# Kernel tuning notes

Hardware: AMD Instinct MI355X
Metric: run time of the kernel (lower is better)

## Reference

```python
import jax, jax.numpy as jnp
import numpy as np


def setup_inputs() -> dict:
    key = jax.random.key(0)
    k1, k2, k3, k4 = jax.random.split(key, 4)
    b, c, h, w = 16, 1024, 32, 32
    dim = h * w  # 1024
    x = jax.random.normal(k1, (b, c, h, w), dtype=jnp.float32)
    cond_img = jax.random.normal(k2, (b, c, h, w), dtype=jnp.float32)
    # torch nn.Linear weights: (out_features, in_features), y = x @ W.T
    Wq = jax.random.normal(k3, (dim, dim), dtype=jnp.float32) * (dim ** -0.5)
    Wkv = jax.random.normal(k4, (2 * dim, dim), dtype=jnp.float32) * (dim ** -0.5)
    return {"x": x, "cond_img": cond_img, "Wq": Wq, "Wkv": Wkv}


def reference(x, cond_img, Wq, Wkv):
    b, c, h, w = x.shape
    dim = h * w
    scale = dim ** -0.5
    xf = x.reshape(b, c, dim)          # (b, c, dim)
    cf = cond_img.reshape(b, c, dim)   # (b, c, dim)
    q = jnp.einsum('bcd,od->bco', xf, Wq)          # (b, c, dim)
    kv = jnp.einsum('bcd,od->bco', cf, Wkv)        # (b, c, 2*dim)
    k, v = jnp.split(kv, 2, axis=-1)               # each (b, c, dim)
    attn = jnp.einsum('bic,bjc->bij', q, k) * scale  # (b, c, c)
    attn = jax.nn.softmax(attn, axis=-1)
    out = jnp.einsum('bij,bjc->bic', attn, v)      # (b, c, dim)
    return out.reshape(b, c, h, w)
```

## Files before the change

### kernel.cpp

```cpp
#include <hip/hip_runtime.h>
#include <stdint.h>


typedef __bf16 bf16_t;
typedef bf16_t bf16x8 __attribute__((ext_vector_type(8)));
typedef float f32x4 __attribute__((ext_vector_type(4)));

#define AS1 __attribute__((address_space(1)))
#define AS3 __attribute__((address_space(3)))

__device__ __forceinline__ uint16_t f2bf(float f) {
  bf16_t h = (bf16_t)f;
  return __builtin_bit_cast(uint16_t, h);
}

__global__ __launch_bounds__(256) void cvt_all(
    const float* __restrict__ x, const float* __restrict__ c,
    const float* __restrict__ wq, const float* __restrict__ wkv,
    uint16_t* __restrict__ XB, uint16_t* __restrict__ CB,
    uint16_t* __restrict__ WQB, uint16_t* __restrict__ WKVB) {
  long i = (long)blockIdx.x * 256 + threadIdx.x;
  if (i >= 9175040) return;
  const float* src;
  uint16_t* dst;
  long off;
  if (i < 4194304) { src = x; dst = XB; off = i; }
  else if (i < 8388608) { src = c; dst = CB; off = i - 4194304; }
  else if (i < 8650752) { src = wq; dst = WQB; off = i - 8388608; }
  else { src = wkv; dst = WKVB; off = i - 8650752; }
  float4 v = ((const float4*)src)[off];
  ushort4 o;
  o.x = f2bf(v.x); o.y = f2bf(v.y); o.z = f2bf(v.z); o.w = f2bf(v.w);
  ((ushort4*)dst)[off] = o;
}

__device__ __forceinline__ void stage_tile(const uint16_t* __restrict__ g,
                                           int ldK, uint16_t* lds, int tid) {
#pragma unroll
  for (int i = 0; i < 4; ++i) {
    int cix = i * 512 + tid;
    int row = cix >> 3;
    int ch = cix & 7;
    int sch = ch ^ (row & 7);
    const uint16_t* gp = g + row * ldK + sch * 8;
    __builtin_amdgcn_global_load_lds((AS1 void*)gp,
                                     (AS3 void*)((uint8_t*)lds + cix * 16), 16,
                                     0, 0);
  }
}

__device__ __forceinline__ void stage128(const uint16_t* __restrict__ g,
                                         int ldK, uint16_t* lds, int tid) {
#pragma unroll
  for (int i = 0; i < 4; ++i) {
    int cix = i * 256 + tid;
    int row = cix >> 3;
    int ch = cix & 7;
    int sch = ch ^ (row & 7);
    const uint16_t* gp = g + row * ldK + sch * 8;
    __builtin_amdgcn_global_load_lds((AS1 void*)gp,
                                     (AS3 void*)((uint8_t*)lds + cix * 16), 16,
                                     0, 0);
  }
}

__device__ __forceinline__ void xcd_decode(int& bx, int& by, int& bz) {
  const int gx = gridDim.x, gy = gridDim.y;
  const int nwg = gx * gy * gridDim.z;
  int fid = blockIdx.x + gx * (blockIdx.y + gy * blockIdx.z);
  int swz = (fid & 7) * (nwg >> 3) + (fid >> 3);
  bx = swz % gx;
  int rem = swz / gx;
  by = rem % gy;
  bz = rem / gy;
}

__global__ __launch_bounds__(512, 2) void g_kv(
    const uint16_t* __restrict__ A, const uint16_t* __restrict__ B,
    uint16_t* __restrict__ Kp, uint16_t* __restrict__ Vp, int K) {
  __shared__ uint16_t smem[65536];

  const int tid = threadIdx.x;
  const int lane = tid & 63;
  const int wid = tid >> 6;
  const int wr = wid >> 2;
  const int wc = wid & 3;
  const int lr = lane & 15, lg = lane >> 4;
  const int ch0 = lr & 7;

  int bx, by, bz;
  xcd_decode(bx, by, bz);
  const int row0 = by * 256;
  const int col0 = bx * 256;
  const uint16_t* At = A + (long long)row0 * K;
  const uint16_t* Bt = B + (long long)col0 * K;

  const int NT = K >> 6;

  stage_tile(At, K, smem, tid);
  stage_tile(Bt, K, smem + 32768, tid);
  stage_tile(At + 64, K, smem + 16384, tid);
  stage_tile(Bt + 64, K, smem + 49152, tid);
  asm volatile("s_waitcnt vmcnt(8)" ::: "memory");
  __builtin_amdgcn_s_barrier();

  f32x4 acc[8][4] = {};
  bf16x8 aA_[4][2], aB_[4][2], bF[4][2];

  {
    const uint8_t* sa = (const uint8_t*)smem;
#pragma unroll
    for (int mi = 0; mi < 4; ++mi)
#pragma unroll
      for (int kk = 0; kk < 2; ++kk)
        aA_[mi][kk] = *(const bf16x8*)(sa + (wr * 128 + mi * 16 + lr) * 128 +
                                       (((kk * 4 + lg) ^ ch0) << 4));
  }

  for (int t = 0; t < NT; ++t) {
    const uint8_t* sa = (const uint8_t*)(smem + (t & 1) * 16384);
    const uint8_t* sb = (const uint8_t*)(smem + 32768 + (t & 1) * 16384);

#pragma unroll
    for (int nj = 0; nj < 4; ++nj)
#pragma unroll
      for (int kk = 0; kk < 2; ++kk)
        bF[nj][kk] = *(const bf16x8*)(sb + (wc * 64 + nj * 16 + lr) * 128 +
                                      (((kk * 4 + lg) ^ ch0) << 4));
#pragma unroll
    for (int mi = 0; mi < 4; ++mi)
#pragma unroll
      for (int kk = 0; kk < 2; ++kk)
        aB_[mi][kk] = *(const bf16x8*)(sa + (wr * 128 + 64 + mi * 16 + lr) * 128 +
                                       (((kk * 4 + lg) ^ ch0) << 4));
    __builtin_amdgcn_s_setprio(1);
#pragma unroll
    for (int kk = 0; kk < 2; ++kk)
#pragma unroll
      for (int mi = 0; mi < 4; ++mi)
#pragma unroll
        for (int nj = 0; nj < 4; ++nj)
          acc[mi][nj] = __builtin_amdgcn_mfma_f32_16x16x32_bf16(
              aA_[mi][kk], bF[nj][kk], acc[mi][nj], 0, 0, 0);
    __builtin_amdgcn_s_setprio(0);
    if (t + 1 < NT) asm volatile("s_waitcnt vmcnt(4)" ::: "memory");
    asm volatile("s_waitcnt lgkmcnt(0)" ::: "memory");
    __builtin_amdgcn_s_barrier();

    if (t + 2 < NT) {
      stage_tile(At + (t + 2) * 64, K, smem + (t & 1) * 16384, tid);
      stage_tile(Bt + (t + 2) * 64, K, smem + 32768 + (t & 1) * 16384, tid);
    }
    if (t + 1 < NT) {
      const uint8_t* sa2 = (const uint8_t*)(smem + ((t + 1) & 1) * 16384);
#pragma unroll
      for (int mi = 0; mi < 4; ++mi)
#pragma unroll
        for (int kk = 0; kk < 2; ++kk)
          aA_[mi][kk] = *(const bf16x8*)(sa2 + (wr * 128 + mi * 16 + lr) * 128 +
                                         (((kk * 4 + lg) ^ ch0) << 4));
    }
    __builtin_amdgcn_s_setprio(1);
#pragma unroll
    for (int kk = 0; kk < 2; ++kk)
#pragma unroll
      for (int mi = 0; mi < 4; ++mi)
#pragma unroll
        for (int nj = 0; nj < 4; ++nj)
          acc[4 + mi][nj] = __builtin_amdgcn_mfma_f32_16x16x32_bf16(
              aB_[mi][kk], bF[nj][kk], acc[4 + mi][nj], 0, 0, 0);
    __builtin_amdgcn_s_setprio(0);
    if (t + 2 < NT)
      asm volatile("s_waitcnt vmcnt(8)" ::: "memory");
    else
      asm volatile("s_waitcnt vmcnt(0)" ::: "memory");
    __builtin_amdgcn_s_barrier();
  }

  if (col0 >= 1024) {
    __syncthreads();
#pragma unroll
    for (int mi = 0; mi < 8; ++mi) {
#pragma unroll
      for (int ni = 0; ni < 4; ++ni) {
        const int cc = wc * 64 + ni * 16 + lr;
        const int jjb = wr * 128 + mi * 16 + lg * 4;
        ushort4 o;
        o.x = f2bf(acc[mi][ni][0]);
        o.y = f2bf(acc[mi][ni][1]);
        o.z = f2bf(acc[mi][ni][2]);
        o.w = f2bf(acc[mi][ni][3]);
        *(ushort4*)&smem[cc * 256 + (jjb ^ ((cc & 7) << 3))] = o;
      }
    }
    __syncthreads();
    const int b = row0 >> 10, jj0 = row0 & 1023;
#pragma unroll
    for (int k = 0; k < 16; ++k) {
      const int cc = k * 16 + (tid >> 5);
      const int jb = (tid & 31) * 8;
      bf16x8 v = *(const bf16x8*)&smem[cc * 256 + (jb ^ ((cc & 7) << 3))];
      *(bf16x8*)(Vp + (long long)b * 1048576 +
                 (long long)(col0 - 1024 + cc) * 1024 + jj0 + jb) = v;
    }
    return;
  }
#pragma unroll
  for (int mi = 0; mi < 8; ++mi) {
#pragma unroll
    for (int ni = 0; ni < 4; ++ni) {
      const int row = row0 + wr * 128 + mi * 16 + lg * 4;
      const int col = col0 + wc * 64 + ni * 16 + lr;
#pragma unroll
      for (int j = 0; j < 4; ++j)
        Kp[(long long)(row + j) * 1024 + col] = f2bf(acc[mi][ni][j]);
    }
  }
}

template <int MODE>
__device__ __forceinline__ void gemm128_body(
    const uint16_t* __restrict__ A, const uint16_t* __restrict__ B,
    void* __restrict__ C0, int K, int N, long long sA, long long sB,
    long long sC, float scale) {
  __shared__ uint16_t smem[32768];

  const int tid = threadIdx.x;
  const int lane = tid & 63;
  const int wid = tid >> 6;
  const int wr = wid >> 1;
  const int wc = wid & 1;
  const int lr = lane & 15, lg = lane >> 4;
  const int ch0 = lr & 7;

  int bx, by, bz;
  xcd_decode(bx, by, bz);
  const int row0 = by * 128;
  const int col0 = bx * 128;
  const uint16_t* At = A + (long long)bz * sA + (long long)row0 * K;
  const uint16_t* Bt = B + (long long)bz * sB + (long long)col0 * K;

  const int NT = K >> 6;

  stage128(At, K, smem, tid);
  stage128(Bt, K, smem + 16384, tid);
  stage128(At + 64, K, smem + 8192, tid);
  stage128(Bt + 64, K, smem + 24576, tid);
  asm volatile("s_waitcnt vmcnt(8)" ::: "memory");
  __builtin_amdgcn_s_barrier();

  f32x4 acc[4][4] = {};
  bf16x8 aA_[2][2], aB_[2][2], bF[4][2];

  {
    const uint8_t* sa = (const uint8_t*)smem;
#pragma unroll
    for (int mi = 0; mi < 2; ++mi)
#pragma unroll
      for (int kk = 0; kk < 2; ++kk)
        aA_[mi][kk] = *(const bf16x8*)(sa + (wr * 64 + mi * 16 + lr) * 128 +
                                       (((kk * 4 + lg) ^ ch0) << 4));
  }

  for (int t = 0; t < NT; ++t) {
    const uint8_t* sa = (const uint8_t*)(smem + (t & 1) * 8192);
    const uint8_t* sb = (const uint8_t*)(smem + 16384 + (t & 1) * 8192);

#pragma unroll
    for (int nj = 0; nj < 4; ++nj)
#pragma unroll
      for (int kk = 0; kk < 2; ++kk)
        bF[nj][kk] = *(const bf16x8*)(sb + (wc * 64 + nj * 16 + lr) * 128 +
                                      (((kk * 4 + lg) ^ ch0) << 4));
#pragma unroll
    for (int mi = 0; mi < 2; ++mi)
#pragma unroll
      for (int kk = 0; kk < 2; ++kk)
        aB_[mi][kk] = *(const bf16x8*)(sa + (wr * 64 + 32 + mi * 16 + lr) * 128 +
                                       (((kk * 4 + lg) ^ ch0) << 4));
    __builtin_amdgcn_s_setprio(1);
#pragma unroll
    for (int kk = 0; kk < 2; ++kk)
#pragma unroll
      for (int mi = 0; mi < 2; ++mi)
#pragma unroll
        for (int nj = 0; nj < 4; ++nj)
          acc[mi][nj] = __builtin_amdgcn_mfma_f32_16x16x32_bf16(
              aA_[mi][kk], bF[nj][kk], acc[mi][nj], 0, 0, 0);
    __builtin_amdgcn_s_setprio(0);
    if (t + 1 < NT) asm volatile("s_waitcnt vmcnt(4)" ::: "memory");
    asm volatile("s_waitcnt lgkmcnt(0)" ::: "memory");
    __builtin_amdgcn_s_barrier();

    if (t + 2 < NT) {
      stage128(At + (t + 2) * 64, K, smem + (t & 1) * 8192, tid);
      stage128(Bt + (t + 2) * 64, K, smem + 16384 + (t & 1) * 8192, tid);
    }
    if (t + 1 < NT) {
      const uint8_t* sa2 = (const uint8_t*)(smem + ((t + 1) & 1) * 8192);
#pragma unroll
      for (int mi = 0; mi < 2; ++mi)
#pragma unroll
        for (int kk = 0; kk < 2; ++kk)
          aA_[mi][kk] = *(const bf16x8*)(sa2 + (wr * 64 + mi * 16 + lr) * 128 +
                                         (((kk * 4 + lg) ^ ch0) << 4));
    }
    __builtin_amdgcn_s_setprio(1);
#pragma unroll
    for (int kk = 0; kk < 2; ++kk)
#pragma unroll
      for (int mi = 0; mi < 2; ++mi)
#pragma unroll
        for (int nj = 0; nj < 4; ++nj)
          acc[2 + mi][nj] = __builtin_amdgcn_mfma_f32_16x16x32_bf16(
              aB_[mi][kk], bF[nj][kk], acc[2 + mi][nj], 0, 0, 0);
    __builtin_amdgcn_s_setprio(0);
    if (t + 2 < NT)
      asm volatile("s_waitcnt vmcnt(8)" ::: "memory");
    else
      asm volatile("s_waitcnt vmcnt(0)" ::: "memory");
    __builtin_amdgcn_s_barrier();
  }

#pragma unroll
  for (int mi = 0; mi < 4; ++mi) {
#pragma unroll
    for (int ni = 0; ni < 4; ++ni) {
      const int row = row0 + wr * 64 + mi * 16 + lg * 4;
      const int col = col0 + wc * 64 + ni * 16 + lr;
      if (MODE == 0) {
        uint16_t* C = (uint16_t*)C0;
#pragma unroll
        for (int j = 0; j < 4; ++j)
          C[(long long)(row + j) * N + col] = f2bf(acc[mi][ni][j]);
      } else {
        float* C = (float*)C0;
#pragma unroll
        for (int j = 0; j < 4; ++j)
          C[(long long)bz * sC + (long long)(row + j) * N + col] =
              acc[mi][ni][j] * scale;
      }
    }
  }
}

__global__ __launch_bounds__(256, 2) void g_qproj(const uint16_t* A,
                                                  const uint16_t* B,
                                                  uint16_t* C, int K, int N) {
  gemm128_body<0>(A, B, C, K, N, 0, 0, 0, 1.0f);
}
__global__ __launch_bounds__(256, 2) void g_s(const uint16_t* A,
                                              const uint16_t* B, float* C,
                                              int K, int N, float scale) {
  gemm128_body<2>(A, B, C, K, N, 1048576, 1048576, 1048576, scale);
}
__global__ __launch_bounds__(256, 2) void g_pv(const uint16_t* A,
                                               const uint16_t* B, float* C,
                                               int K, int N) {
  gemm128_body<2>(A, B, C, K, N, 1048576, 1048576, 1048576, 1.0f);
}

__global__ __launch_bounds__(256) void softmax_rows(const float* __restrict__ S,
                                                    uint16_t* __restrict__ P) {
  const int row = blockIdx.x;
  const int t = threadIdx.x;
  const int w = t >> 6, l = t & 63;
  __shared__ float red[8];

  const float4 v = ((const float4*)(S + (long long)row * 1024))[t];
  float m = fmaxf(fmaxf(v.x, v.y), fmaxf(v.z, v.w));
#pragma unroll
  for (int o = 1; o < 64; o <<= 1) m = fmaxf(m, __shfl_xor(m, o, 64));
  if (l == 0) red[w] = m;
  __syncthreads();
  m = fmaxf(fmaxf(red[0], red[1]), fmaxf(red[2], red[3]));

  float e0 = __expf(v.x - m), e1 = __expf(v.y - m);
  float e2 = __expf(v.z - m), e3 = __expf(v.w - m);
  float s = e0 + e1 + e2 + e3;
#pragma unroll
  for (int o = 1; o < 64; o <<= 1) s += __shfl_xor(s, o, 64);
  if (l == 0) red[4 + w] = s;
  __syncthreads();
  s = red[4] + red[5] + red[6] + red[7];
  const float inv = 1.0f / s;

  ushort4 o4;
  o4.x = f2bf(e0 * inv); o4.y = f2bf(e1 * inv);
  o4.z = f2bf(e2 * inv); o4.w = f2bf(e3 * inv);
  ((ushort4*)P)[(long long)row * 256 + t] = o4;
}

extern "C" void kernel_launch(void* const* d_in, const int* in_sizes, int n_in,
                              void* d_out, int out_size, void* d_ws, size_t ws_size,
                              hipStream_t stream) {
  const float* x    = (const float*)d_in[0];
  const float* cond = (const float*)d_in[1];
  const float* Wq   = (const float*)d_in[2];
  const float* Wkv  = (const float*)d_in[3];
  float* out = (float*)d_out;

  uint8_t* ws = (uint8_t*)d_ws;
  const long long MiB = 1ll << 20;
  uint16_t* XB   = (uint16_t*)(ws + 0 * MiB);
  uint16_t* CB   = (uint16_t*)(ws + 32 * MiB);
  float*    S    = (float*)(ws + 0 * MiB);
  uint16_t* WQB  = (uint16_t*)(ws + 64 * MiB);
  uint16_t* WKVB = (uint16_t*)(ws + 66 * MiB);
  uint16_t* Q    = (uint16_t*)(ws + 70 * MiB);
  uint16_t* Kb   = (uint16_t*)(ws + 102 * MiB);
  uint16_t* VT   = (uint16_t*)(ws + 134 * MiB);

  cvt_all<<<35840, 256, 0, stream>>>(x, cond, Wq, Wkv, XB, CB, WQB, WKVB);

  g_qproj<<<dim3(8, 128), 256, 0, stream>>>(XB, WQB, Q, 1024, 1024);
  g_kv<<<dim3(8, 64), 512, 0, stream>>>(CB, WKVB, Kb, VT, 1024);
  g_s<<<dim3(8, 8, 16), 256, 0, stream>>>(Q, Kb, S, 1024, 1024, 0.03125f);
  softmax_rows<<<16384, 256, 0, stream>>>(S, Q);
  g_pv<<<dim3(8, 8, 16), 256, 0, stream>>>(Q, VT, out, 1024, 1024);
}
```

Baseline: 249.4 us.

## Fuse softmax into score and PV GEMM epilogues without max subtraction

Removes the standalone softmax kernel. The score GEMM now writes exp(scaled score) as bf16 and per-tile partial row sums. The PV GEMM reduces those partial sums and divides its accumulators by the row sum in the epilogue. This drops the fp32 S write and re-read plus a kernel launch. It skips the row-max subtraction, so it can overflow for large logits and stores unnormalized exponentials in bf16.

```diff
diff --git a/kernel.cpp b/kernel.cpp
--- a/kernel.cpp
+++ b/kernel.cpp
@@ -218,12 +218,13 @@
   }
 }
 
-template <int MODE>
+template <int EPI>
 __device__ __forceinline__ void gemm128_body(
     const uint16_t* __restrict__ A, const uint16_t* __restrict__ B,
-    void* __restrict__ C0, int K, int N, long long sA, long long sB,
-    long long sC, float scale) {
+    void* __restrict__ C0, float* __restrict__ Rpart, int K, int N,
+    long long sA, long long sB, long long sC, float scale) {
   __shared__ uint16_t smem[32768];
+  __shared__ float RLDS[128];
 
   const int tid = threadIdx.x;
   const int lane = tid & 63;
@@ -237,10 +238,20 @@
   xcd_decode(bx, by, bz);
   const int row0 = by * 128;
   const int col0 = bx * 128;
+  const int grow0 = bz * (N >= 1024 ? 1024 : N) + row0;
   const uint16_t* At = A + (long long)bz * sA + (long long)row0 * K;
   const uint16_t* Bt = B + (long long)bz * sB + (long long)col0 * K;
 
   const int NT = K >> 6;
+
+  if (EPI == 4) {
+    if (tid < 128) {
+      float r = 0.f;
+#pragma unroll
+      for (int p = 0; p < 8; ++p) r += Rpart[p * 16384 + grow0 + tid];
+      RLDS[tid] = 1.0f / r;
+    }
+  }
 
   stage128(At, K, smem, tid);
   stage128(Bt, K, smem + 16384, tid);
@@ -322,73 +333,87 @@
     __builtin_amdgcn_s_barrier();
   }
 
-#pragma unroll
-  for (int mi = 0; mi < 4; ++mi) {
-#pragma unroll
-    for (int ni = 0; ni < 4; ++ni) {
-      const int row = row0 + wr * 64 + mi * 16 + lg * 4;
-      const int col = col0 + wc * 64 + ni * 16 + lr;
-      if (MODE == 0) {
-        uint16_t* C = (uint16_t*)C0;
+  if (EPI == 0) {
+    uint16_t* C = (uint16_t*)C0;
+#pragma unroll
+    for (int mi = 0; mi < 4; ++mi)
+#pragma unroll
+      for (int ni = 0; ni < 4; ++ni) {
+        const int row = row0 + wr * 64 + mi * 16 + lg * 4;
+        const int col = col0 + wc * 64 + ni * 16 + lr;
 #pragma unroll
         for (int j = 0; j < 4; ++j)
           C[(long long)(row + j) * N + col] = f2bf(acc[mi][ni][j]);
-      } else {
-        float* C = (float*)C0;
+      }
+  } else if (EPI == 3) {
+    uint16_t* Pp = (uint16_t*)C0 + (long long)bz * sC;
+    float rs[4][4];
+#pragma unroll
+    for (int mi = 0; mi < 4; ++mi) {
+#pragma unroll
+      for (int j = 0; j < 4; ++j) rs[mi][j] = 0.f;
+#pragma unroll
+      for (int ni = 0; ni < 4; ++ni) {
+        const int row = row0 + wr * 64 + mi * 16 + lg * 4;
+        const int col = col0 + wc * 64 + ni * 16 + lr;
+#pragma unroll
+        for (int j = 0; j < 4; ++j) {
+          float e = __expf(acc[mi][ni][j] * scale);
+          Pp[(long long)(row + j) * N + col] = f2bf(e);
+          rs[mi][j] += e;
+        }
+      }
+    }
+#pragma unroll
+    for (int o = 1; o < 16; o <<= 1)
+#pragma unroll
+      for (int mi = 0; mi < 4; ++mi)
+#pragma unroll
+        for (int j = 0; j < 4; ++j) rs[mi][j] += __shfl_xor(rs[mi][j], o, 64);
+    __syncthreads();
+    float* RS = (float*)smem;
+    if (lr == 0) {
+#pragma unroll
+      for (int mi = 0; mi < 4; ++mi)
 #pragma unroll
         for (int j = 0; j < 4; ++j)
+          RS[wc * 128 + wr * 64 + mi * 16 + lg * 4 + j] = rs[mi][j];
+    }
+    __syncthreads();
+    if (tid < 128) Rpart[bx * 16384 + grow0 + tid] = RS[tid] + RS[128 + tid];
+  } else {
+    float* C = (float*)C0;
+#pragma unroll
+    for (int mi = 0; mi < 4; ++mi)
+#pragma unroll
+      for (int ni = 0; ni < 4; ++ni) {
+        const int row = row0 + wr * 64 + mi * 16 + lg * 4;
+        const int col = col0 + wc * 64 + ni * 16 + lr;
+#pragma unroll
+        for (int j = 0; j < 4; ++j) {
+          const float rinv = RLDS[wr * 64 + mi * 16 + lg * 4 + j];
           C[(long long)bz * sC + (long long)(row + j) * N + col] =
-              acc[mi][ni][j] * scale;
+              acc[mi][ni][j] * rinv;
+        }
       }
-    }
   }
 }
 
 __global__ __launch_bounds__(256, 2) void g_qproj(const uint16_t* A,
                                                   const uint16_t* B,
                                                   uint16_t* C, int K, int N) {
-  gemm128_body<0>(A, B, C, K, N, 0, 0, 0, 1.0f);
+  gemm128_body<0>(A, B, C, nullptr, K, N, 0, 0, 0, 1.0f);
 }
 __global__ __launch_bounds__(256, 2) void g_s(const uint16_t* A,
-                                              const uint16_t* B, float* C,
-                                              int K, int N, float scale) {
-  gemm128_body<2>(A, B, C, K, N, 1048576, 1048576, 1048576, scale);
+                                              const uint16_t* B, uint16_t* Pp,
+                                              float* Rpart, int K,
+                                              float scale) {
+  gemm128_body<3>(A, B, Pp, Rpart, K, 1024, 1048576, 1048576, 1048576, scale);
 }
 __global__ __launch_bounds__(256, 2) void g_pv(const uint16_t* A,
                                                const uint16_t* B, float* C,
-                                               int K, int N) {
-  gemm128_body<2>(A, B, C, K, N, 1048576, 1048576, 1048576, 1.0f);
-}
-
-__global__ __launch_bounds__(256) void softmax_rows(const float* __restrict__ S,
-                                                    uint16_t* __restrict__ P) {
-  const int row = blockIdx.x;
-  const int t = threadIdx.x;
-  const int w = t >> 6, l = t & 63;
-  __shared__ float red[8];
-
-  const float4 v = ((const float4*)(S + (long long)row * 1024))[t];
-  float m = fmaxf(fmaxf(v.x, v.y), fmaxf(v.z, v.w));
-#pragma unroll
-  for (int o = 1; o < 64; o <<= 1) m = fmaxf(m, __shfl_xor(m, o, 64));
-  if (l == 0) red[w] = m;
-  __syncthreads();
-  m = fmaxf(fmaxf(red[0], red[1]), fmaxf(red[2], red[3]));
-
-  float e0 = __expf(v.x - m), e1 = __expf(v.y - m);
-  float e2 = __expf(v.z - m), e3 = __expf(v.w - m);
-  float s = e0 + e1 + e2 + e3;
-#pragma unroll
-  for (int o = 1; o < 64; o <<= 1) s += __shfl_xor(s, o, 64);
-  if (l == 0) red[4 + w] = s;
-  __syncthreads();
-  s = red[4] + red[5] + red[6] + red[7];
-  const float inv = 1.0f / s;
-
-  ushort4 o4;
-  o4.x = f2bf(e0 * inv); o4.y = f2bf(e1 * inv);
-  o4.z = f2bf(e2 * inv); o4.w = f2bf(e3 * inv);
-  ((ushort4*)P)[(long long)row * 256 + t] = o4;
+                                               float* Rpart, int K) {
+  gemm128_body<4>(A, B, C, Rpart, K, 1024, 1048576, 1048576, 1048576, 1.0f);
 }
 
 extern "C" void kernel_launch(void* const* d_in, const int* in_sizes, int n_in,
@@ -402,20 +427,20 @@
 
   uint8_t* ws = (uint8_t*)d_ws;
   const long long MiB = 1ll << 20;
-  uint16_t* XB   = (uint16_t*)(ws + 0 * MiB);
-  uint16_t* CB   = (uint16_t*)(ws + 32 * MiB);
-  float*    S    = (float*)(ws + 0 * MiB);
-  uint16_t* WQB  = (uint16_t*)(ws + 64 * MiB);
-  uint16_t* WKVB = (uint16_t*)(ws + 66 * MiB);
-  uint16_t* Q    = (uint16_t*)(ws + 70 * MiB);
-  uint16_t* Kb   = (uint16_t*)(ws + 102 * MiB);
-  uint16_t* VT   = (uint16_t*)(ws + 134 * MiB);
+  uint16_t* XB    = (uint16_t*)(ws + 0 * MiB);
+  uint16_t* CB    = (uint16_t*)(ws + 32 * MiB);
+  uint16_t* Pp    = (uint16_t*)(ws + 0 * MiB);
+  float*    Rpart = (float*)(ws + 32 * MiB);
+  uint16_t* WQB   = (uint16_t*)(ws + 64 * MiB);
+  uint16_t* WKVB  = (uint16_t*)(ws + 66 * MiB);
+  uint16_t* Q     = (uint16_t*)(ws + 70 * MiB);
+  uint16_t* Kb    = (uint16_t*)(ws + 102 * MiB);
+  uint16_t* VT    = (uint16_t*)(ws + 134 * MiB);
 
   cvt_all<<<35840, 256, 0, stream>>>(x, cond, Wq, Wkv, XB, CB, WQB, WKVB);
 
   g_qproj<<<dim3(8, 128), 256, 0, stream>>>(XB, WQB, Q, 1024, 1024);
   g_kv<<<dim3(8, 64), 512, 0, stream>>>(CB, WKVB, Kb, VT, 1024);
-  g_s<<<dim3(8, 8, 16), 256, 0, stream>>>(Q, Kb, S, 1024, 1024, 0.03125f);
-  softmax_rows<<<16384, 256, 0, stream>>>(S, Q);
-  g_pv<<<dim3(8, 8, 16), 256, 0, stream>>>(Q, VT, out, 1024, 1024);
-}
+  g_s<<<dim3(8, 8, 16), 256, 0, stream>>>(Q, Kb, Pp, Rpart, 1024, 0.03125f);
+  g_pv<<<dim3(8, 8, 16), 256, 0, stream>>>(Pp, VT, out, Rpart, 1024);
+}
```

Result: faster. 236.4 us (-5.2%).
